# Kernel tuning notes

Hardware: AMD Instinct MI355X
Metric: run time of the kernel (lower is better)

The kernel has to match this reference:

```python
import jax, jax.numpy as jnp
import numpy as np

# config
B, V, S, D = 2, 8, 256, 2048
NH, NKV, KVR = 32, 8, 2
HD = D // NH            # 64
G = NH // NKV           # GQA group size = 4
INIT = 0.02


def _neighbor_idx():
    # replicates generate_neighbor: left neighbors (i-half..i-1) then right (i+1..i+half), circular
    half = KVR // 2
    offsets = np.concatenate([np.arange(-half, 0), np.arange(1, half + 1)])
    return (np.arange(V)[:, None] + offsets[None, :]) % V  # [V, KVR]


def setup_inputs() -> dict:
    key = jax.random.key(0)
    k1, k2, k3, k4 = jax.random.split(key, 4)
    x = jax.random.normal(k1, (B, V, S, D), jnp.float32)
    wq = jax.random.normal(k2, (D, NH * HD), jnp.float32) * INIT
    wkv = jax.random.normal(k3, (D, 2 * NKV * HD), jnp.float32) * INIT
    wo = jax.random.normal(k4, (D, D), jnp.float32) * INIT
    return {"x": x, "wq": wq, "wkv": wkv, "wo": wo}


def reference(x, wq, wkv, wo):
    b, v, s, d = x.shape
    idx = _neighbor_idx()  # [V, KVR] static

    # Q projection: [b, v, s, NH*HD]
    xq = (x @ wq).reshape(b, v, s, NKV, G, HD)  # grouped-query layout (kv head, group)

    # neighbor gather: [b, v, KVR, s, d] -> [b, v, KVR*s, d]
    x_kv = x[:, idx].reshape(b, v, KVR * s, d)
    kv = x_kv @ wkv
    xk, xv = jnp.split(kv, 2, axis=-1)
    xk = xk.reshape(b, v, KVR * s, NKV, HD)
    xv = xv.reshape(b, v, KVR * s, NKV, HD)

    # grouped-query SDPA (no mask, eval mode): avoids materializing repeated K/V
    scale = 1.0 / jnp.sqrt(jnp.asarray(HD, x.dtype))
    scores = jnp.einsum('bvsngh,bvtnh->bvngst', xq, xk) * scale  # [b,v,NKV,G,s,KVR*s]
    attn = jax.nn.softmax(scores, axis=-1)
    out = jnp.einsum('bvngst,bvtnh->bvsngh', attn, xv).reshape(b, v, s, d)
    return out @ wo
```

## Files before the change

### kernel.cpp

```cpp
#include <hip/hip_runtime.h>
#include <stdint.h>

typedef unsigned short u16;
typedef unsigned int   u32;
typedef short short8 __attribute__((ext_vector_type(8)));
typedef float f32x4  __attribute__((ext_vector_type(4)));

__device__ __forceinline__ u16 f2bf(float f){
  u32 u = __builtin_bit_cast(u32, f);
  u32 r = (u + 0x7FFFu + ((u >> 16) & 1u)) >> 16;
  return (u16)r;
}
__device__ __forceinline__ u32 packbf(float a, float b){
  return (u32)f2bf(a) | ((u32)f2bf(b) << 16);
}
__device__ __forceinline__ void gload16(const u16* g, u16* l){
  __builtin_amdgcn_global_load_lds((const __attribute__((address_space(1))) void*)g,
                                   (__attribute__((address_space(3))) void*)l, 16, 0, 0);
}

__global__ __launch_bounds__(256) void k_cvt_bf16(const float* __restrict__ x,
                                                  u16* __restrict__ y, int n8){
  int i = blockIdx.x * 256 + threadIdx.x;
  if (i >= n8) return;
  const float4* p = (const float4*)x + (size_t)i * 2;
  float4 a = p[0], b = p[1];
  short8 o;
  o[0] = f2bf(a.x); o[1] = f2bf(a.y); o[2] = f2bf(a.z); o[3] = f2bf(a.w);
  o[4] = f2bf(b.x); o[5] = f2bf(b.y); o[6] = f2bf(b.z); o[7] = f2bf(b.w);
  *(short8*)(y + (size_t)i * 8) = o;
}

__global__ __launch_bounds__(256) void k_transpose_w(const float* __restrict__ in,
                                                     u16* __restrict__ out, int R, int C){
  __shared__ float tile[32][33];
  int nc = C >> 5;
  int cb = blockIdx.x % nc, rb = blockIdx.x / nc;
  int tx = threadIdx.x & 31, ty = threadIdx.x >> 5;
#pragma unroll
  for (int i = 0; i < 4; ++i){
    int r = rb * 32 + ty + i * 8;
    tile[ty + i * 8][tx] = in[(size_t)r * C + cb * 32 + tx];
  }
  __syncthreads();
#pragma unroll
  for (int i = 0; i < 4; ++i){
    int c = cb * 32 + ty + i * 8;
    out[(size_t)c * R + rb * 32 + tx] = f2bf(tile[tx][ty + i * 8]);
  }
}

template<int BN, int NFRAG, typename CT>
__global__ __launch_bounds__(512, 1) void k_gemm8(const u16* __restrict__ A,
                                                  const u16* __restrict__ Bt,
                                                  CT* __restrict__ C,
                                                  int N, int K){
  constexpr int SZA = 256 * 64;
  constexpr int SZB = BN * 64;
  constexpr int SZ  = SZA + SZB;
  constexpr int BSLICES = SZB / 1024;
  constexpr int WT_N = BN / 4;
  __shared__ u16 lds[4 * SZ / 2];

  int tid = threadIdx.x, lane = tid & 63, wid = tid >> 6;
  int l16 = lane & 15, g4 = lane >> 4;
  int wm = wid >> 2, wn = wid & 3;
  int bid = blockIdx.x;
  int wg = (bid & 7) * 32 + (bid >> 3);
  int bm = wg >> 4, bn = wg & 15;

  const u16* baseA = A  + (size_t)(bm * 256) * K;
  const u16* baseB = Bt + (size_t)(bn * BN) * K;

  int aq[2], ag[2];
#pragma unroll
  for (int i = 0; i < 2; ++i){
    int q = (i * 8 + wid) * 1024 + lane * 16;
    int row = q >> 6, c = q & 63;
    int cs = c ^ ((row & 3) << 4);
    aq[i] = q; ag[i] = row * K + (cs >> 1);
  }
  int bq[2], bg[2];
#pragma unroll
  for (int j = 0; j < 2; ++j){
    int slice = wid + j * 8;
    int q = slice * 1024 + lane * 16;
    int row = q >> 6, c = q & 63;
    int cs = c ^ ((row & 3) << 4);
    bq[j] = q; bg[j] = row * K + (cs >> 1);
  }

  auto stageA = [&](int kt3, int i){
    int buf = kt3 & 3;
    gload16(baseA + ag[i] + kt3 * 32, (u16*)((char*)lds + buf * SZ + aq[i]));
  };
  auto stageB = [&](int kt3, int j){
    int buf = kt3 & 3;
    gload16(baseB + bg[j] + kt3 * 32, (u16*)((char*)lds + buf * SZ + SZA + bq[j]));
  };

  f32x4 zero4 = {0.f, 0.f, 0.f, 0.f};
  f32x4 acc[8][NFRAG];
#pragma unroll
  for (int i = 0; i < 8; ++i)
#pragma unroll
    for (int j = 0; j < NFRAG; ++j) acc[i][j] = zero4;

  int NK = K >> 5;
  for (int p = 0; p < 3; ++p){
    stageA(p, 0); stageB(p, 0);
    stageA(p, 1);
    if (wid < BSLICES - 8) stageB(p, 1);
  }

  int xr = (l16 & 3) << 4;
  for (int kt = 0; kt < NK; ++kt){
    if (kt < NK - 2)       asm volatile("s_waitcnt vmcnt(6)" ::: "memory");
    else if (kt == NK - 2) asm volatile("s_waitcnt vmcnt(3)" ::: "memory");
    else                   asm volatile("s_waitcnt vmcnt(0)" ::: "memory");
    __builtin_amdgcn_s_barrier();
    __builtin_amdgcn_sched_barrier(0);

    const char* Ab = (const char*)lds + (kt & 3) * SZ;
    const char* Bb = Ab + SZA;
    bool st = (kt + 3 < NK);

    short8 bfr[NFRAG];
#pragma unroll
    for (int nf = 0; nf < NFRAG; ++nf){
      int row = wn * WT_N + nf * 16 + l16;
      bfr[nf] = *(const short8*)(Bb + row * 64 + ((g4 * 16) ^ xr));
    }
    short8 af[4];
#pragma unroll
    for (int mf = 0; mf < 4; ++mf){
      int row = wm * 128 + mf * 16 + l16;
      af[mf] = *(const short8*)(Ab + row * 64 + ((g4 * 16) ^ xr));
    }
    if (st){ stageA(kt + 3, 0); stageB(kt + 3, 0); }
    __builtin_amdgcn_s_setprio(1);
#pragma unroll
    for (int mf = 0; mf < 4; ++mf)
#pragma unroll
      for (int nf = 0; nf < NFRAG; ++nf)
        acc[mf][nf] = __builtin_amdgcn_mfma_f32_16x16x32_bf16(af[mf], bfr[nf], acc[mf][nf], 0, 0, 0);
    __builtin_amdgcn_s_setprio(0);
    __builtin_amdgcn_s_barrier();
    __builtin_amdgcn_sched_barrier(0);

#pragma unroll
    for (int mf = 0; mf < 4; ++mf){
      int row = wm * 128 + 64 + mf * 16 + l16;
      af[mf] = *(const short8*)(Ab + row * 64 + ((g4 * 16) ^ xr));
    }
    if (st){ stageA(kt + 3, 1); if (wid < BSLICES - 8) stageB(kt + 3, 1); }
    __builtin_amdgcn_s_setprio(1);
#pragma unroll
    for (int mf = 0; mf < 4; ++mf)
#pragma unroll
      for (int nf = 0; nf < NFRAG; ++nf)
        acc[4 + mf][nf] = __builtin_amdgcn_mfma_f32_16x16x32_bf16(af[mf], bfr[nf], acc[4 + mf][nf], 0, 0, 0);
    __builtin_amdgcn_s_setprio(0);
  }

#pragma unroll
  for (int mf = 0; mf < 8; ++mf)
#pragma unroll
    for (int nf = 0; nf < NFRAG; ++nf)
#pragma unroll
      for (int r = 0; r < 4; ++r){
        int row = bm * 256 + wm * 128 + mf * 16 + g4 * 4 + r;
        int col = bn * BN + wn * WT_N + nf * 16 + l16;
        float vv = acc[mf][nf][r];
        if constexpr (sizeof(CT) == 2) C[(size_t)row * N + col] = (CT)f2bf(vv);
        else                           C[(size_t)row * N + col] = (CT)vv;
      }
}

__global__ __launch_bounds__(256) void k_vt(const u16* __restrict__ c1, u16* __restrict__ vt){
  __shared__ u16 tile[64][72];
  int bid = blockIdx.x;
  int st = bid & 3, n = (bid >> 2) & 7, bv = bid >> 5;
  int t = threadIdx.x;
  int sr = t >> 2, sc = t & 3;
  const u16* src = c1 + (size_t)(bv * 256 + st * 64 + sr) * 3072 + 2560 + n * 64 + sc * 16;
  short8 a = *(const short8*)src;
  short8 b = *(const short8*)(src + 8);
  *(short8*)&tile[sr][sc * 16]     = a;
  *(short8*)&tile[sr][sc * 16 + 8] = b;
  __syncthreads();
  int h = t >> 2, c2 = t & 3;
  short8 o0, o1;
#pragma unroll
  for (int j = 0; j < 8; ++j) o0[j] = (short)tile[c2 * 16 + j][h];
#pragma unroll
  for (int j = 0; j < 8; ++j) o1[j] = (short)tile[c2 * 16 + 8 + j][h];
  u16* dst = vt + (size_t)((bv * 8 + n) * 64 + h) * 256 + st * 64 + c2 * 16;
  *(short8*)dst       = o0;
  *(short8*)(dst + 8) = o1;
}

__global__ __launch_bounds__(256, 2) void k_attn(const u16* __restrict__ c1,
                                                 const u16* __restrict__ vt,
                                                 u16* __restrict__ att){
  __shared__ u16 Klds[64][72];
  __shared__ u16 Vlds[64][72];
  __shared__ u16 Plds[4][16][72];
  int bid = blockIdx.x;
  int qt = bid & 3, n = (bid >> 2) & 7, v = (bid >> 5) & 7, b = bid >> 8;
  int tid = threadIdx.x;
  int g = tid >> 6, lane = tid & 63, l16 = lane & 15, g4 = lane >> 4;
  int bv = b * 8 + v;
  int rowQ = bv * 256 + qt * 64;
  int qcol = n * 256 + g * 64;
  const float SC2 = 0.18033688011112042f;

  short8 qf[4][2];
#pragma unroll
  for (int qi = 0; qi < 4; ++qi)
#pragma unroll
    for (int kk = 0; kk < 2; ++kk)
      qf[qi][kk] = *(const short8*)(c1 + (size_t)(rowQ + qi * 16 + l16) * 3072
                                     + qcol + kk * 32 + g4 * 8);

  f32x4 zero4 = {0.f, 0.f, 0.f, 0.f};
  f32x4 O[4][4];
#pragma unroll
  for (int i = 0; i < 4; ++i)
#pragma unroll
    for (int j = 0; j < 4; ++j) O[i][j] = zero4;
  float m2[4]   = {-3.0e38f, -3.0e38f, -3.0e38f, -3.0e38f};
  float lsum[4] = {0.f, 0.f, 0.f, 0.f};

  int sr = tid >> 2, sc = tid & 3;
  short8 k0, k1, v0, v1;
  {
    int vn = (v + 7) & 7;
    const u16* ks = c1 + (size_t)((b * 8 + vn) * 256 + sr) * 3072 + 2048 + n * 64 + sc * 16;
    k0 = *(const short8*)ks; k1 = *(const short8*)(ks + 8);
    const u16* vs = vt + (size_t)(((b * 8 + vn) * 8 + n) * 64 + sr) * 256 + sc * 16;
    v0 = *(const short8*)vs; v1 = *(const short8*)(vs + 8);
  }

  for (int ti = 0; ti < 8; ++ti){
    __syncthreads();
    *(short8*)&Klds[sr][sc * 16]     = k0;
    *(short8*)&Klds[sr][sc * 16 + 8] = k1;
    *(short8*)&Vlds[sr][sc * 16]     = v0;
    *(short8*)&Vlds[sr][sc * 16 + 8] = v1;
    __syncthreads();
    if (ti < 7){
      int tn = ti + 1;
      int vn = (tn < 4) ? ((v + 7) & 7) : ((v + 1) & 7);
      int tb = (tn & 3) * 64;
      const u16* ks = c1 + (size_t)((b * 8 + vn) * 256 + tb + sr) * 3072 + 2048 + n * 64 + sc * 16;
      k0 = *(const short8*)ks; k1 = *(const short8*)(ks + 8);
      const u16* vs = vt + (size_t)(((b * 8 + vn) * 8 + n) * 64 + sr) * 256 + tb + sc * 16;
      v0 = *(const short8*)vs; v1 = *(const short8*)(vs + 8);
    }
    short8 kf[4][2], vf[2][4];
#pragma unroll
    for (int kt = 0; kt < 4; ++kt)
#pragma unroll
      for (int ks = 0; ks < 2; ++ks)
        kf[kt][ks] = *(const short8*)&Klds[kt * 16 + l16][ks * 32 + g4 * 8];
#pragma unroll
    for (int ks = 0; ks < 2; ++ks)
#pragma unroll
      for (int hi = 0; hi < 4; ++hi)
        vf[ks][hi] = *(const short8*)&Vlds[hi * 16 + l16][ks * 32 + g4 * 8];

#pragma unroll
    for (int qi = 0; qi < 4; ++qi){
      f32x4 sa[4];
#pragma unroll
      for (int kt = 0; kt < 4; ++kt){
        sa[kt] = zero4;
#pragma unroll
        for (int ks = 0; ks < 2; ++ks)
          sa[kt] = __builtin_amdgcn_mfma_f32_16x16x32_bf16(kf[kt][ks], qf[qi][ks], sa[kt], 0, 0, 0);
      }
      float smax = -3.0e38f;
#pragma unroll
      for (int kt = 0; kt < 4; ++kt)
#pragma unroll
        for (int r = 0; r < 4; ++r){
          float s = sa[kt][r] * SC2;
          sa[kt][r] = s;
          smax = fmaxf(smax, s);
        }
      smax = fmaxf(smax, __shfl_xor(smax, 16));
      smax = fmaxf(smax, __shfl_xor(smax, 32));
      float mnew  = fmaxf(m2[qi], smax);
      float alpha = exp2f(m2[qi] - mnew);
      m2[qi] = mnew;
      float psum = 0.f;
      u32 w[4][2];
#pragma unroll
      for (int kt = 0; kt < 4; ++kt){
        float p0 = exp2f(sa[kt][0] - mnew);
        float p1 = exp2f(sa[kt][1] - mnew);
        float p2 = exp2f(sa[kt][2] - mnew);
        float p3 = exp2f(sa[kt][3] - mnew);
        psum += (p0 + p1) + (p2 + p3);
        w[kt][0] = packbf(p0, p1);
        w[kt][1] = packbf(p2, p3);
      }
      psum += __shfl_xor(psum, 16);
      psum += __shfl_xor(psum, 32);
      lsum[qi] = lsum[qi] * alpha + psum;
      u32* prow = (u32*)&Plds[g][l16][0];
#pragma unroll
      for (int kt = 0; kt < 4; ++kt){
        prow[kt * 8 + g4 * 2]     = w[kt][0];
        prow[kt * 8 + g4 * 2 + 1] = w[kt][1];
      }
      float ab[4];
#pragma unroll
      for (int r = 0; r < 4; ++r) ab[r] = __shfl(alpha, g4 * 4 + r);
#pragma unroll
      for (int hi = 0; hi < 4; ++hi)
#pragma unroll
        for (int r = 0; r < 4; ++r) O[qi][hi][r] *= ab[r];
      short8 pa[2];
#pragma unroll
      for (int ks = 0; ks < 2; ++ks)
        pa[ks] = *(const short8*)&Plds[g][l16][ks * 32 + g4 * 8];
#pragma unroll
      for (int hi = 0; hi < 4; ++hi)
#pragma unroll
        for (int ks = 0; ks < 2; ++ks)
          O[qi][hi] = __builtin_amdgcn_mfma_f32_16x16x32_bf16(pa[ks], vf[ks][hi], O[qi][hi], 0, 0, 0);
    }
  }
#pragma unroll
  for (int qi = 0; qi < 4; ++qi){
    float lb[4];
#pragma unroll
    for (int r = 0; r < 4; ++r) lb[r] = 1.0f / __shfl(lsum[qi], g4 * 4 + r);
#pragma unroll
    for (int hi = 0; hi < 4; ++hi)
#pragma unroll
      for (int r = 0; r < 4; ++r){
        int row = rowQ + qi * 16 + g4 * 4 + r;
        int col = qcol + hi * 16 + l16;
        att[(size_t)row * 2048 + col] = f2bf(O[qi][hi][r] * lb[r]);
      }
  }
}

extern "C" void kernel_launch(void* const* d_in, const int* in_sizes, int n_in,
                              void* d_out, int out_size, void* d_ws, size_t ws_size,
                              hipStream_t stream){
  const float* x   = (const float*)d_in[0];
  const float* wq  = (const float*)d_in[1];
  const float* wkv = (const float*)d_in[2];
  const float* wo  = (const float*)d_in[3];
  float* out = (float*)d_out;
  char* ws = (char*)d_ws;

  u16* x_bf  = (u16*)(ws);
  u16* wqkvt = (u16*)(ws + 16777216);
  u16* wot   = (u16*)(ws + 29360128);
  u16* c1    = (u16*)(ws + 37748736);
  u16* vt    = (u16*)(ws + 62914560);
  u16* att   = x_bf;

  k_cvt_bf16<<<4096, 256, 0, stream>>>(x, x_bf, 1048576);
  k_transpose_w<<<4096, 256, 0, stream>>>(wq,  wqkvt,               2048, 2048);
  k_transpose_w<<<2048, 256, 0, stream>>>(wkv, wqkvt + 2048 * 2048, 2048, 1024);
  k_transpose_w<<<4096, 256, 0, stream>>>(wo,  wot,                 2048, 2048);
  k_gemm8<192, 3, u16><<<256, 512, 0, stream>>>(x_bf, wqkvt, c1, 3072, 2048);
  k_vt<<<512, 256, 0, stream>>>(c1, vt);
  k_attn<<<512, 256, 0, stream>>>(c1, vt, att);
  k_gemm8<128, 2, float><<<256, 512, 0, stream>>>(att, wot, out, 2048, 2048);
}
```

Measured before the change: 169.4 us.

## Restructure GEMM to double-buffered BK=64 tiles with interleaved LDS reads

```diff
diff --git a/kernel.cpp b/kernel.cpp
--- a/kernel.cpp
+++ b/kernel.cpp
@@ -50,17 +50,16 @@
   }
 }
 
-template<int BN, int NFRAG, typename CT>
-__global__ __launch_bounds__(512, 1) void k_gemm8(const u16* __restrict__ A,
-                                                  const u16* __restrict__ Bt,
-                                                  CT* __restrict__ C,
-                                                  int N, int K){
-  constexpr int SZA = 256 * 64;
-  constexpr int SZB = BN * 64;
+template<int BN, int NFRAG, int BLOADS, typename CT>
+__global__ __launch_bounds__(512, 2) void k_gemm8p(const u16* __restrict__ A,
+                                                   const u16* __restrict__ Bt,
+                                                   CT* __restrict__ C,
+                                                   int N, int K){
+  constexpr int SZA = 256 * 128;
+  constexpr int SZB = BN * 128;
   constexpr int SZ  = SZA + SZB;
-  constexpr int BSLICES = SZB / 1024;
   constexpr int WT_N = BN / 4;
-  __shared__ u16 lds[4 * SZ / 2];
+  __shared__ char lds[2 * SZ];
 
   int tid = threadIdx.x, lane = tid & 63, wid = tid >> 6;
   int l16 = lane & 15, g4 = lane >> 4;
@@ -72,31 +71,39 @@
   const u16* baseA = A  + (size_t)(bm * 256) * K;
   const u16* baseB = Bt + (size_t)(bn * BN) * K;
 
-  int aq[2], ag[2];
-#pragma unroll
-  for (int i = 0; i < 2; ++i){
-    int q = (i * 8 + wid) * 1024 + lane * 16;
-    int row = q >> 6, c = q & 63;
-    int cs = c ^ ((row & 3) << 4);
-    aq[i] = q; ag[i] = row * K + (cs >> 1);
-  }
-  int bq[2], bg[2];
-#pragma unroll
-  for (int j = 0; j < 2; ++j){
-    int slice = wid + j * 8;
-    int q = slice * 1024 + lane * 16;
-    int row = q >> 6, c = q & 63;
-    int cs = c ^ ((row & 3) << 4);
-    bq[j] = q; bg[j] = row * K + (cs >> 1);
-  }
-
-  auto stageA = [&](int kt3, int i){
-    int buf = kt3 & 3;
-    gload16(baseA + ag[i] + kt3 * 32, (u16*)((char*)lds + buf * SZ + aq[i]));
+  int aLds[4], aG[4];
+#pragma unroll
+  for (int i = 0; i < 4; ++i){
+    int q = (wid * 4 + i) * 1024 + lane * 16;
+    int row = q >> 7, c = q & 127;
+    int cs = c ^ ((row & 7) << 4);
+    aLds[i] = q; aG[i] = row * K + (cs >> 1);
+  }
+  int bLds[BLOADS], bG[BLOADS];
+#pragma unroll
+  for (int j = 0; j < BLOADS; ++j){
+    int q = (wid * BLOADS + j) * 1024 + lane * 16;
+    int row = q >> 7, c = q & 127;
+    int cs = c ^ ((row & 7) << 4);
+    bLds[j] = q; bG[j] = row * K + (cs >> 1);
+  }
+  auto stageA = [&](int t){
+    char* dst = lds + (t & 1) * SZ;
+#pragma unroll
+    for (int i = 0; i < 4; ++i) gload16(baseA + aG[i] + t * 64, (u16*)(dst + aLds[i]));
   };
-  auto stageB = [&](int kt3, int j){
-    int buf = kt3 & 3;
-    gload16(baseB + bg[j] + kt3 * 32, (u16*)((char*)lds + buf * SZ + SZA + bq[j]));
+  auto stageB = [&](int t){
+    char* dst = lds + (t & 1) * SZ + SZA;
+#pragma unroll
+    for (int j = 0; j < BLOADS; ++j) gload16(baseB + bG[j] + t * 64, (u16*)(dst + bLds[j]));
+  };
+  auto rdA = [&](const char* Ab, int m, int ks){
+    int row = wm * 128 + m * 16 + l16;
+    return *(const short8*)(Ab + row * 128 + ((ks * 64 + g4 * 16) ^ ((row & 7) << 4)));
+  };
+  auto rdB = [&](const char* Bb, int nf, int ks){
+    int row = wn * WT_N + nf * 16 + l16;
+    return *(const short8*)(Bb + row * 128 + ((ks * 64 + g4 * 16) ^ ((row & 7) << 4)));
   };
 
   f32x4 zero4 = {0.f, 0.f, 0.f, 0.f};
@@ -106,61 +113,62 @@
 #pragma unroll
     for (int j = 0; j < NFRAG; ++j) acc[i][j] = zero4;
 
-  int NK = K >> 5;
-  for (int p = 0; p < 3; ++p){
-    stageA(p, 0); stageB(p, 0);
-    stageA(p, 1);
-    if (wid < BSLICES - 8) stageB(p, 1);
-  }
-
-  int xr = (l16 & 3) << 4;
+  int NK = K >> 6;
+  stageA(0); stageB(0);
+  asm volatile("s_waitcnt vmcnt(0)" ::: "memory");
+
   for (int kt = 0; kt < NK; ++kt){
-    if (kt < NK - 2)       asm volatile("s_waitcnt vmcnt(6)" ::: "memory");
-    else if (kt == NK - 2) asm volatile("s_waitcnt vmcnt(3)" ::: "memory");
-    else                   asm volatile("s_waitcnt vmcnt(0)" ::: "memory");
+    const char* Ab = lds + (kt & 1) * SZ;
+    const char* Bb = Ab + SZA;
+    bool st = (kt + 1 < NK);
     __builtin_amdgcn_s_barrier();
-    __builtin_amdgcn_sched_barrier(0);
-
-    const char* Ab = (const char*)lds + (kt & 3) * SZ;
-    const char* Bb = Ab + SZA;
-    bool st = (kt + 3 < NK);
-
-    short8 bfr[NFRAG];
-#pragma unroll
-    for (int nf = 0; nf < NFRAG; ++nf){
-      int row = wn * WT_N + nf * 16 + l16;
-      bfr[nf] = *(const short8*)(Bb + row * 64 + ((g4 * 16) ^ xr));
-    }
-    short8 af[4];
-#pragma unroll
-    for (int mf = 0; mf < 4; ++mf){
-      int row = wm * 128 + mf * 16 + l16;
-      af[mf] = *(const short8*)(Ab + row * 64 + ((g4 * 16) ^ xr));
-    }
-    if (st){ stageA(kt + 3, 0); stageB(kt + 3, 0); }
+    short8 bf0[NFRAG], a0[4], a1[4], bf1[NFRAG], a2[4], a3[4];
+#pragma unroll
+    for (int nf = 0; nf < NFRAG; ++nf) bf0[nf] = rdB(Bb, nf, 0);
+#pragma unroll
+    for (int m = 0; m < 4; ++m) a0[m] = rdA(Ab, m, 0);
+    if (st) stageA(kt + 1);
+#pragma unroll
+    for (int m = 0; m < 4; ++m) a1[m] = rdA(Ab, 4 + m, 0);
     __builtin_amdgcn_s_setprio(1);
 #pragma unroll
-    for (int mf = 0; mf < 4; ++mf)
+    for (int m = 0; m < 4; ++m)
 #pragma unroll
       for (int nf = 0; nf < NFRAG; ++nf)
-        acc[mf][nf] = __builtin_amdgcn_mfma_f32_16x16x32_bf16(af[mf], bfr[nf], acc[mf][nf], 0, 0, 0);
+        acc[m][nf] = __builtin_amdgcn_mfma_f32_16x16x32_bf16(a0[m], bf0[nf], acc[m][nf], 0, 0, 0);
     __builtin_amdgcn_s_setprio(0);
     __builtin_amdgcn_s_barrier();
-    __builtin_amdgcn_sched_barrier(0);
-
-#pragma unroll
-    for (int mf = 0; mf < 4; ++mf){
-      int row = wm * 128 + 64 + mf * 16 + l16;
-      af[mf] = *(const short8*)(Ab + row * 64 + ((g4 * 16) ^ xr));
-    }
-    if (st){ stageA(kt + 3, 1); if (wid < BSLICES - 8) stageB(kt + 3, 1); }
+    if (st) stageB(kt + 1);
+#pragma unroll
+    for (int nf = 0; nf < NFRAG; ++nf) bf1[nf] = rdB(Bb, nf, 1);
+#pragma unroll
+    for (int m = 0; m < 4; ++m) a2[m] = rdA(Ab, m, 1);
     __builtin_amdgcn_s_setprio(1);
 #pragma unroll
-    for (int mf = 0; mf < 4; ++mf)
+    for (int m = 0; m < 4; ++m)
 #pragma unroll
       for (int nf = 0; nf < NFRAG; ++nf)
-        acc[4 + mf][nf] = __builtin_amdgcn_mfma_f32_16x16x32_bf16(af[mf], bfr[nf], acc[4 + mf][nf], 0, 0, 0);
+        acc[4 + m][nf] = __builtin_amdgcn_mfma_f32_16x16x32_bf16(a1[m], bf0[nf], acc[4 + m][nf], 0, 0, 0);
     __builtin_amdgcn_s_setprio(0);
+    __builtin_amdgcn_s_barrier();
+#pragma unroll
+    for (int m = 0; m < 4; ++m) a3[m] = rdA(Ab, 4 + m, 1);
+    __builtin_amdgcn_s_setprio(1);
+#pragma unroll
+    for (int m = 0; m < 4; ++m)
+#pragma unroll
+      for (int nf = 0; nf < NFRAG; ++nf)
+        acc[m][nf] = __builtin_amdgcn_mfma_f32_16x16x32_bf16(a2[m], bf1[nf], acc[m][nf], 0, 0, 0);
+    __builtin_amdgcn_s_setprio(0);
+    __builtin_amdgcn_s_barrier();
+    __builtin_amdgcn_s_setprio(1);
+#pragma unroll
+    for (int m = 0; m < 4; ++m)
+#pragma unroll
+      for (int nf = 0; nf < NFRAG; ++nf)
+        acc[4 + m][nf] = __builtin_amdgcn_mfma_f32_16x16x32_bf16(a3[m], bf1[nf], acc[4 + m][nf], 0, 0, 0);
+    __builtin_amdgcn_s_setprio(0);
+    if (st) asm volatile("s_waitcnt vmcnt(0)" ::: "memory");
   }
 
 #pragma unroll
@@ -370,8 +378,8 @@
   k_transpose_w<<<4096, 256, 0, stream>>>(wq,  wqkvt,               2048, 2048);
   k_transpose_w<<<2048, 256, 0, stream>>>(wkv, wqkvt + 2048 * 2048, 2048, 1024);
   k_transpose_w<<<4096, 256, 0, stream>>>(wo,  wot,                 2048, 2048);
-  k_gemm8<192, 3, u16><<<256, 512, 0, stream>>>(x_bf, wqkvt, c1, 3072, 2048);
+  k_gemm8p<192, 3, 3, u16><<<256, 512, 0, stream>>>(x_bf, wqkvt, c1, 3072, 2048);
   k_vt<<<512, 256, 0, stream>>>(c1, vt);
   k_attn<<<512, 256, 0, stream>>>(c1, vt, att);
-  k_gemm8<128, 2, float><<<256, 512, 0, stream>>>(att, wot, out, 2048, 2048);
-}
+  k_gemm8p<128, 2, 2, float><<<256, 512, 0, stream>>>(att, wot, out, 2048, 2048);
+}
```

Result: faster. 160.6 us (-5.2%).
